# Performance work log

Measured on AMD Instinct MI355X. Metric: run time of the kernel, lower is better.

Reference implementation:

```python
import jax, jax.numpy as jnp
import numpy as np

B, S, E, F, R, T = 2, 2048, 768, 3072, 4, 128
H = 12  # num_heads
HD = E // H
HID = 128  # lora_mlp_dim


def _lin(key, out_f, in_f):
    bound = 1.0 / np.sqrt(in_f)
    return jax.random.uniform(key, (out_f, in_f), jnp.float32, -bound, bound)


def _bias(key, out_f, in_f):
    bound = 1.0 / np.sqrt(in_f)
    return jax.random.uniform(key, (out_f,), jnp.float32, -bound, bound)


def setup_inputs() -> dict:
    key = jax.random.key(0)
    ks = jax.random.split(key, 20)
    return {
        "src": jax.random.normal(ks[0], (B, S, E), jnp.float32),
        "task_embedding": jax.random.normal(ks[1], (B, S, T), jnp.float32),
        "norm1_w": jnp.ones((E,), jnp.float32),
        "norm2_w": jnp.ones((E,), jnp.float32),
        "in_proj_w": _lin(ks[2], 3 * E, E),      # MHA qkv, bias=False
        "out_proj_w": _lin(ks[3], E, E),          # MHA out, bias=False
        "ffn1_w": _lin(ks[4], F, E), "ffn1_b": _bias(ks[5], F, E),
        "ffn2_w": _lin(ks[6], E, F), "ffn2_b": _bias(ks[7], E, F),
        "hA_w1": _lin(ks[8], HID, T), "hA_b1": _bias(ks[9], HID, T),
        "hA_w2": _lin(ks[10], F * R, HID), "hA_b2": _bias(ks[11], F * R, HID),
        "hB_w1": _lin(ks[12], HID, T), "hB_b1": _bias(ks[13], HID, T),
        "hB_w2": _lin(ks[14], R * E, HID), "hB_b2": _bias(ks[15], R * E, HID),
    }


def _rmsnorm(x, w):
    eps = jnp.finfo(x.dtype).eps
    return x * jax.lax.rsqrt(jnp.mean(x * x, axis=-1, keepdims=True) + eps) * w


def reference(src, task_embedding, norm1_w, norm2_w, in_proj_w, out_proj_w,
              ffn1_w, ffn1_b, ffn2_w, ffn2_b,
              hA_w1, hA_b1, hA_w2, hA_b2, hB_w1, hB_b1, hB_w2, hB_b2):
    # --- self-attention block (pre-RMSNorm) ---
    x = _rmsnorm(src, norm1_w)
    qkv = jnp.einsum('bse,fe->bsf', x, in_proj_w)  # [B,S,3E]
    q, k, v = jnp.split(qkv, 3, axis=-1)
    q = q.reshape(B, S, H, HD).transpose(0, 2, 1, 3)
    k = k.reshape(B, S, H, HD).transpose(0, 2, 1, 3)
    v = v.reshape(B, S, H, HD).transpose(0, 2, 1, 3)
    scores = jnp.einsum('bhqd,bhkd->bhqk', q, k) / jnp.sqrt(jnp.float32(HD))
    attn = jax.nn.softmax(scores, axis=-1)
    ctx = jnp.einsum('bhqk,bhkd->bhqd', attn, v)
    ctx = ctx.transpose(0, 2, 1, 3).reshape(B, S, E)
    attn_out = jnp.einsum('bse,fe->bsf', ctx, out_proj_w)
    src = src + attn_out

    # --- FFN block with per-token hypernetwork LoRA on linear1 ---
    x = _rmsnorm(src, norm2_w)
    # hypernetwork: MLP(task) -> per-token A [F,R], B [R,E]
    hA = jax.nn.relu(jnp.einsum('bst,ht->bsh', task_embedding, hA_w1) + hA_b1)
    A_params = (jnp.einsum('bsh,fh->bsf', hA, hA_w2) + hA_b2).reshape(B, S, F, R)
    hB = jax.nn.relu(jnp.einsum('bst,ht->bsh', task_embedding, hB_w1) + hB_b1)
    B_params = (jnp.einsum('bsh,fh->bsf', hB, hB_w2) + hB_b2).reshape(B, S, R, E)

    base = jnp.einsum('bse,fe->bsf', x, ffn1_w) + ffn1_b  # [B,S,F]
    inter = jnp.einsum('bse,bsre->bsr', x, B_params)       # [B,S,R]
    adapt = jnp.einsum('bsr,bsfr->bsf', inter, A_params)   # [B,S,F]
    h = jax.nn.relu(base + adapt)
    out2 = jnp.einsum('bsf,ef->bse', h, ffn2_w) + ffn2_b
    return src + out2
```

## Files before the change

### kernel.cpp

```cpp
#include <hip/hip_runtime.h>
#include <math.h>

#define NB 2
#define NS 2048
#define NE 768
#define NF 3072
#define NHEAD 12
#define NTOK 4096
#define LDW 1344

typedef __bf16 bf16;
typedef __bf16 bf16x4 __attribute__((ext_vector_type(4)));
typedef __bf16 bf16x8 __attribute__((ext_vector_type(8)));
typedef float  f32x4  __attribute__((ext_vector_type(4)));

__device__ __forceinline__ f32x4 mfma_bf16(bf16x8 a, bf16x8 b, f32x4 c) {
  return __builtin_amdgcn_mfma_f32_16x16x32_bf16(a, b, c, 0, 0, 0);
}

__device__ __forceinline__ float fast_exp2(float x) {
#if __has_builtin(__builtin_amdgcn_exp2f)
  return __builtin_amdgcn_exp2f(x);
#else
  return exp2f(x);
#endif
}

__device__ __forceinline__ void glds16(const void* g, void* l) {
  __builtin_amdgcn_global_load_lds((const __attribute__((address_space(1))) void*)g,
                                   (__attribute__((address_space(3))) void*)l,
                                   16, 0, 0);
}

__device__ __forceinline__ void swz_xy(int& bx, int& by) {
  int gx = gridDim.x;
  int i = by*gx + bx;
  int xcd = i & 7, s = i >> 3;
  int bands = gridDim.y >> 3;
  by = xcd*bands + s / gx;
  bx = s % gx;
}

__global__ void prep_kernel(const float* __restrict__ in_proj, const float* __restrict__ out_proj,
                            const float* __restrict__ ffn1_w, const float* __restrict__ ffn1_b,
                            const float* __restrict__ ffn2_w,
                            const float* __restrict__ hA_w1, const float* __restrict__ hA_b1,
                            const float* __restrict__ hA_w2, const float* __restrict__ hA_b2,
                            const float* __restrict__ hB_w1, const float* __restrict__ hB_b1,
                            const float* __restrict__ hB_w2,
                            const float* __restrict__ task,
                            bf16* __restrict__ Wqkv, bf16* __restrict__ Wo, bf16* __restrict__ W2,
                            bf16* __restrict__ W1ab, float* __restrict__ b1ab,
                            bf16* __restrict__ WBp, bf16* __restrict__ Wc,
                            bf16* __restrict__ task_bf)
{
  __shared__ float tb[64*130];
  int stride = gridDim.x * blockDim.x;
  int t0 = blockIdx.x * blockDim.x + threadIdx.x;
  const float QS = 0.125f * 1.44269504088896f;
  for (int i = t0; i < (2304*768)/4; i += stride) {
    float4 v = ((const float4*)in_proj)[i];
    float sc = (i < (768*768)/4) ? QS : 1.0f;
    *(bf16x4*)(Wqkv + i*4) = (bf16x4){(bf16)(v.x*sc), (bf16)(v.y*sc), (bf16)(v.z*sc), (bf16)(v.w*sc)};
  }
  for (int i = t0; i < (768*768)/4; i += stride) {
    float4 v = ((const float4*)out_proj)[i];
    *(bf16x4*)(Wo + i*4) = (bf16x4){(bf16)v.x, (bf16)v.y, (bf16)v.z, (bf16)v.w};
  }
  for (int i = t0; i < (768*3072)/4; i += stride) {
    float4 v = ((const float4*)ffn2_w)[i];
    *(bf16x4*)(W2 + i*4) = (bf16x4){(bf16)v.x, (bf16)v.y, (bf16)v.z, (bf16)v.w};
  }
  for (int i = t0; i < (NTOK*128)/4; i += stride) {
    float4 v = ((const float4*)task)[i];
    *(bf16x4*)(task_bf + i*4) = (bf16x4){(bf16)v.x, (bf16)v.y, (bf16)v.z, (bf16)v.w};
  }
  for (int i = t0; i < 256*128;  i += stride)
    W1ab[i] = (bf16)(i < 128*128 ? hA_w1[i] : hB_w1[i - 128*128]);
  for (int i = t0; i < 256; i += stride) b1ab[i] = (i < 128) ? hA_b1[i] : hB_b1[i-128];

  for (int j0 = blockIdx.x*64; j0 < 3072; j0 += gridDim.x*64) {
    __syncthreads();
    for (int i = threadIdx.x; i < 64*128; i += 256) {
      int jr = i >> 7, hh = i & 127;
      tb[jr*130 + hh] = hB_w2[(long)(j0 + jr)*128 + hh];
    }
    __syncthreads();
    int r = j0 / 768, e0 = j0 % 768;
    for (int i = threadIdx.x; i < 128*64; i += 256) {
      int hh = i >> 6, jr = i & 63;
      WBp[(long)(r*128 + hh)*768 + e0 + jr] = (bf16)tb[jr*130 + hh];
    }
  }

  for (int f = blockIdx.x; f < 3072; f += gridDim.x) {
    const float* hrow = hA_w2 + (long)f*512;
    bf16* wrow = Wc + (long)f*LDW;
    for (int c = threadIdx.x; c < 768; c += 256) wrow[c] = (bf16)ffn1_w[(long)f*768 + c];
    for (int i = threadIdx.x; i < 512; i += 256) {
      int r = i >> 7, h = i & 127;
      wrow[768 + h*4 + r] = (bf16)hrow[i];
    }
    if (threadIdx.x < 4)        wrow[1280 + threadIdx.x] = (bf16)hA_b2[f*4 + threadIdx.x];
    else if (threadIdx.x == 4)  wrow[1284] = (bf16)ffn1_b[f];
    else if (threadIdx.x < 64)  wrow[1280 + threadIdx.x] = (bf16)0.f;
  }
}

__global__ __launch_bounds__(256) void rmsnorm_k(const float* __restrict__ x,
                                                 const float* __restrict__ w,
                                                 bf16* __restrict__ out, int ld_out)
{
  __shared__ float red[4];
  long t = blockIdx.x;
  const float* xr = x + t*NE;
  float ss = 0.f;
  #pragma unroll
  for (int i = 0; i < 3; i++) { float v = xr[threadIdx.x + i*256]; ss += v*v; }
  #pragma unroll
  for (int d = 1; d < 64; d <<= 1) ss += __shfl_xor(ss, d, 64);
  if ((threadIdx.x & 63) == 0) red[threadIdx.x >> 6] = ss;
  __syncthreads();
  float tot = red[0] + red[1] + red[2] + red[3];
  float scale = rsqrtf(tot * (1.f/768.f) + 1.1920928955078125e-07f);
  #pragma unroll
  for (int i = 0; i < 3; i++) {
    int idx = threadIdx.x + i*256;
    out[t*ld_out + idx] = (bf16)(xr[idx] * scale * w[idx]);
  }
}

template<typename OutT, bool RELU, bool BIAS, bool RES>
__global__ __launch_bounds__(256) void gemm_bt_sw(const bf16* __restrict__ A,
                                                  const bf16* __restrict__ Bm,
                                                  OutT* __restrict__ C,
                                                  const float* __restrict__ bias,
                                                  const float* __restrict__ res,
                                                  int K, int lda, int ldb, int ldc)
{
  __shared__ bf16 As[2][128*32];
  __shared__ bf16 Bs[2][128*32];
  const int tid = threadIdx.x;
  int bx = blockIdx.x, by = blockIdx.y;
  swz_xy(bx, by);
  const int m0 = by * 128;
  const int n0 = bx * 128;
  const int w = tid >> 6, lane = tid & 63;
  const int quad = lane >> 4, l16 = lane & 15;
  const int wy = w >> 1, wx = w & 1;

  f32x4 acc[4][4];
  #pragma unroll
  for (int i = 0; i < 4; i++)
    #pragma unroll
    for (int j = 0; j < 4; j++) acc[i][j] = (f32x4){0.f,0.f,0.f,0.f};

  const int i0 = tid, i1 = tid + 256;
  const int R0 = i0 >> 3, cc0 = (i0 & 7) ^ (R0 & 7), r0 = 2*R0 + (cc0 >> 2), ch0 = (cc0 & 3) * 8;
  const int R1 = i1 >> 3, cc1 = (i1 & 7) ^ (R1 & 7), r1 = 2*R1 + (cc1 >> 2), ch1 = (cc1 & 3) * 8;
  const bf16* pA0 = A  + (long)(m0 + r0)*lda + ch0;
  const bf16* pA1 = A  + (long)(m0 + r1)*lda + ch1;
  const bf16* pB0 = Bm + (long)(n0 + r0)*ldb + ch0;
  const bf16* pB1 = Bm + (long)(n0 + r1)*ldb + ch1;
  auto stage = [&](int buf) {
    glds16(pA0, (void*)(&As[buf][i0*8]));
    glds16(pA1, (void*)(&As[buf][i1*8]));
    glds16(pB0, (void*)(&Bs[buf][i0*8]));
    glds16(pB1, (void*)(&Bs[buf][i1*8]));
    pA0 += 32; pA1 += 32; pB0 += 32; pB1 += 32;
  };

  stage(0);
  __builtin_amdgcn_s_waitcnt(0);
  __syncthreads();

  const int Rh = l16 >> 1;
  const int ppq = ((l16 & 1) << 2) | quad;
  const int jfr = ppq ^ Rh;
  const int nsteps = K >> 5;
  for (int s = 0; s < nsteps; ++s) {
    const int cur = s & 1;
    if (s + 1 < nsteps) stage(cur ^ 1);

    bf16x8 af[4], bfr[4];
    #pragma unroll
    for (int mi = 0; mi < 4; ++mi)
      af[mi] = *(const bf16x8*)(&As[cur][(wy*32 + mi*8 + Rh)*64 + jfr*8]);
    #pragma unroll
    for (int ni = 0; ni < 4; ++ni)
      bfr[ni] = *(const bf16x8*)(&Bs[cur][(wx*32 + ni*8 + Rh)*64 + jfr*8]);
    #pragma unroll
    for (int mi = 0; mi < 4; ++mi)
      #pragma unroll
      for (int ni = 0; ni < 4; ++ni)
        acc[mi][ni] = mfma_bf16(af[mi], bfr[ni], acc[mi][ni]);

    __builtin_amdgcn_s_waitcnt(0);
    __syncthreads();
  }

  #pragma unroll
  for (int mi = 0; mi < 4; ++mi)
    #pragma unroll
    for (int ni = 0; ni < 4; ++ni) {
      int col = n0 + wx*64 + ni*16 + l16;
      #pragma unroll
      for (int r = 0; r < 4; ++r) {
        long row = m0 + wy*64 + mi*16 + quad*4 + r;
        float v = acc[mi][ni][r];
        if (BIAS) v += bias[col];
        if (RES)  v += res[row*ldc + col];
        if (RELU) v = v > 0.f ? v : 0.f;
        C[row*ldc + col] = (OutT)v;
      }
    }
}

template<typename OutT, bool RELU, bool BIAS, bool RES>
__global__ __launch_bounds__(256) void gemm64(const bf16* __restrict__ A,
                                              const bf16* __restrict__ Bm,
                                              OutT* __restrict__ C,
                                              const float* __restrict__ bias,
                                              const float* __restrict__ res,
                                              int K, int lda, int ldb, int ldc)
{
  __shared__ bf16 As[2][64*64];
  __shared__ bf16 Bs[2][64*64];
  const int tid = threadIdx.x;
  int bx = blockIdx.x, by = blockIdx.y;
  swz_xy(bx, by);
  const int m0 = by * 64, n0 = bx * 64;
  const int w = tid >> 6, lane = tid & 63;
  const int quad = lane >> 4, l16 = lane & 15;
  const int wy = w >> 1, wx = w & 1;
  const int sw = l16 & 7;

  f32x4 acc[2][2];
  #pragma unroll
  for (int i = 0; i < 2; i++)
    #pragma unroll
    for (int j = 0; j < 2; j++) acc[i][j] = (f32x4){0.f,0.f,0.f,0.f};

  const int c0 = tid, c1 = tid + 256;
  const int r0 = c0 >> 3, g0 = ((c0 & 7) ^ (r0 & 7)) * 8;
  const int r1 = c1 >> 3, g1 = ((c1 & 7) ^ (r1 & 7)) * 8;
  const bf16* pA0 = A  + (long)(m0 + r0)*lda + g0;
  const bf16* pA1 = A  + (long)(m0 + r1)*lda + g1;
  const bf16* pB0 = Bm + (long)(n0 + r0)*ldb + g0;
  const bf16* pB1 = Bm + (long)(n0 + r1)*ldb + g1;
  auto stage = [&](int buf) {
    glds16(pA0, (void*)(&As[buf][c0*8]));
    glds16(pA1, (void*)(&As[buf][c1*8]));
    glds16(pB0, (void*)(&Bs[buf][c0*8]));
    glds16(pB1, (void*)(&Bs[buf][c1*8]));
    pA0 += 64; pA1 += 64; pB0 += 64; pB1 += 64;
  };

  stage(0);
  __builtin_amdgcn_s_waitcnt(0);
  __syncthreads();

  const int nsteps = K >> 6;
  for (int s = 0; s < nsteps; ++s) {
    const int cur = s & 1;
    if (s + 1 < nsteps) stage(cur ^ 1);

    bf16x8 af[2][2], bfr[2][2];
    #pragma unroll
    for (int mi = 0; mi < 2; ++mi)
      #pragma unroll
      for (int kb = 0; kb < 2; ++kb)
        af[mi][kb] = *(const bf16x8*)(&As[cur][(wy*32 + mi*16 + l16)*64 + (((kb*4 + quad) ^ sw))*8]);
    #pragma unroll
    for (int ni = 0; ni < 2; ++ni)
      #pragma unroll
      for (int kb = 0; kb < 2; ++kb)
        bfr[ni][kb] = *(const bf16x8*)(&Bs[cur][(wx*32 + ni*16 + l16)*64 + (((kb*4 + quad) ^ sw))*8]);
    #pragma unroll
    for (int kb = 0; kb < 2; ++kb)
      #pragma unroll
      for (int mi = 0; mi < 2; ++mi)
        #pragma unroll
        for (int ni = 0; ni < 2; ++ni)
          acc[mi][ni] = mfma_bf16(af[mi][kb], bfr[ni][kb], acc[mi][ni]);

    __builtin_amdgcn_s_waitcnt(0);
    __syncthreads();
  }

  #pragma unroll
  for (int mi = 0; mi < 2; ++mi)
    #pragma unroll
    for (int ni = 0; ni < 2; ++ni) {
      int col = n0 + wx*32 + ni*16 + l16;
      #pragma unroll
      for (int r = 0; r < 4; ++r) {
        long row = m0 + wy*32 + mi*16 + quad*4 + r;
        float v = acc[mi][ni][r];
        if (BIAS) v += bias[col];
        if (RES)  v += res[row*ldc + col];
        if (RELU) v = v > 0.f ? v : 0.f;
        C[row*ldc + col] = (OutT)v;
      }
    }
}

__global__ __launch_bounds__(256) void gemm_qkv64(const bf16* __restrict__ A,
                                                  const bf16* __restrict__ Bm,
                                                  bf16* __restrict__ Qkv,
                                                  bf16* __restrict__ Vt)
{
  __shared__ bf16 As[2][64*64];
  __shared__ bf16 Bs[2][64*64];
  const int tid = threadIdx.x;
  int bx = blockIdx.x, by = blockIdx.y;
  swz_xy(bx, by);
  const int m0 = by * 64, n0 = bx * 64;
  const int w = tid >> 6, lane = tid & 63;
  const int quad = lane >> 4, l16 = lane & 15;
  const int wy = w >> 1, wx = w & 1;
  const int sw = l16 & 7;

  f32x4 acc[2][2];
  #pragma unroll
  for (int i = 0; i < 2; i++)
    #pragma unroll
    for (int j = 0; j < 2; j++) acc[i][j] = (f32x4){0.f,0.f,0.f,0.f};

  const int c0 = tid, c1 = tid + 256;
  const int r0 = c0 >> 3, g0 = ((c0 & 7) ^ (r0 & 7)) * 8;
  const int r1 = c1 >> 3, g1 = ((c1 & 7) ^ (r1 & 7)) * 8;
  const bf16* pA0 = A  + (long)(m0 + r0)*768 + g0;
  const bf16* pA1 = A  + (long)(m0 + r1)*768 + g1;
  const bf16* pB0 = Bm + (long)(n0 + r0)*768 + g0;
  const bf16* pB1 = Bm + (long)(n0 + r1)*768 + g1;
  auto stage = [&](int buf) {
    glds16(pA0, (void*)(&As[buf][c0*8]));
    glds16(pA1, (void*)(&As[buf][c1*8]));
    glds16(pB0, (void*)(&Bs[buf][c0*8]));
    glds16(pB1, (void*)(&Bs[buf][c1*8]));
    pA0 += 64; pA1 += 64; pB0 += 64; pB1 += 64;
  };

  stage(0);
  __builtin_amdgcn_s_waitcnt(0);
  __syncthreads();

  for (int s = 0; s < 12; ++s) {
    const int cur = s & 1;
    if (s + 1 < 12) stage(cur ^ 1);

    bf16x8 af[2][2], bfr[2][2];
    #pragma unroll
    for (int mi = 0; mi < 2; ++mi)
      #pragma unroll
      for (int kb = 0; kb < 2; ++kb)
        af[mi][kb] = *(const bf16x8*)(&As[cur][(wy*32 + mi*16 + l16)*64 + (((kb*4 + quad) ^ sw))*8]);
    #pragma unroll
    for (int ni = 0; ni < 2; ++ni)
      #pragma unroll
      for (int kb = 0; kb < 2; ++kb)
        bfr[ni][kb] = *(const bf16x8*)(&Bs[cur][(wx*32 + ni*16 + l16)*64 + (((kb*4 + quad) ^ sw))*8]);
    #pragma unroll
    for (int kb = 0; kb < 2; ++kb)
      #pragma unroll
      for (int mi = 0; mi < 2; ++mi)
        #pragma unroll
        for (int ni = 0; ni < 2; ++ni)
          acc[mi][ni] = mfma_bf16(af[mi][kb], bfr[ni][kb], acc[mi][ni]);

    __builtin_amdgcn_s_waitcnt(0);
    __syncthreads();
  }

  const int bb = m0 >> 11;
  #pragma unroll
  for (int mi = 0; mi < 2; ++mi)
    #pragma unroll
    for (int ni = 0; ni < 2; ++ni) {
      int col = n0 + wx*32 + ni*16 + l16;
      #pragma unroll
      for (int r = 0; r < 4; ++r) {
        long row = m0 + wy*32 + mi*16 + quad*4 + r;
        bf16 v = (bf16)acc[mi][ni][r];
        if (col < 1536) {
          Qkv[row*2304 + col] = v;
        } else {
          int vc = col - 1536;
          int hh = vc >> 6, d = vc & 63;
          long srow = row & (NS-1);
          Vt[((long)(bb*NHEAD + hh)*64 + d)*NS + srow] = v;
        }
      }
    }
}

__global__ __launch_bounds__(128) void flash_attn(const bf16* __restrict__ Qkv,
                                                  const bf16* __restrict__ Vt,
                                                  bf16* __restrict__ Ctx)
{
  __shared__ bf16 Ks[2][64*64];
  __shared__ bf16 Vs[2][64*64];

  const int tid = threadIdx.x;
  const int w = tid >> 6, lane = tid & 63;
  const int quad = lane >> 4, l16 = lane & 15;
  const int bh = blockIdx.y;
  const int b = bh / NHEAD, h = bh % NHEAD;
  const int q0 = blockIdx.x * 64;

  bf16x8 qf[2][2];
  #pragma unroll
  for (int mi = 0; mi < 2; ++mi) {
    const long tq = (long)(b*NS + q0 + w*32 + mi*16 + l16);
    qf[mi][0] = *(const bf16x8*)(Qkv + tq*2304 + h*64 + quad*8);
    qf[mi][1] = *(const bf16x8*)(Qkv + tq*2304 + h*64 + 32 + quad*8);
  }

  bf16x8 ones;
  #pragma unroll
  for (int j = 0; j < 8; ++j) ones[j] = (bf16)1.0f;

  f32x4 o[2][4];
  f32x4 o5[2];
  #pragma unroll
  for (int mi = 0; mi < 2; ++mi) {
    o5[mi] = (f32x4){0.f,0.f,0.f,0.f};
    #pragma unroll
    for (int i = 0; i < 4; i++) o[mi][i] = (f32x4){0.f,0.f,0.f,0.f};
  }

  const bf16* kp[4];
  const bf16* vp[4];
  int cc[4];
  #pragma unroll
  for (int i = 0; i < 4; ++i) {
    int c = tid + i*128;
    cc[i] = c;
    int r = c >> 3, g = ((c & 7) ^ (r & 7)) * 8;
    kp[i] = Qkv + (long)(b*NS + r)*2304 + 768 + h*64 + g;
    vp[i] = Vt + ((long)bh*64 + r)*NS + g;
  }
  auto stage = [&](int buf) {
    #pragma unroll
    for (int i = 0; i < 4; ++i) {
      glds16(kp[i], (void*)(&Ks[buf][cc[i]*8]));
      glds16(vp[i], (void*)(&Vs[buf][cc[i]*8]));
      kp[i] += 64*2304; vp[i] += 64;
    }
  };

  auto body = [&](int cur) {
    bf16x8 kfr[4][2];
    #pragma unroll
    for (int nt = 0; nt < 4; ++nt)
      #pragma unroll
      for (int kb = 0; kb < 2; ++kb)
        kfr[nt][kb] = *(const bf16x8*)(&Ks[cur][(nt*16 + l16)*64 + (((kb*4 + quad) ^ (l16 & 7)))*8]);

    bf16x8 pf[2][2];
    #pragma unroll
    for (int mi = 0; mi < 2; ++mi) {
      f32x4 s[4];
      #pragma unroll
      for (int nt = 0; nt < 4; ++nt) {
        s[nt] = (f32x4){0.f,0.f,0.f,0.f};
        #pragma unroll
        for (int kb = 0; kb < 2; ++kb)
          s[nt] = mfma_bf16(kfr[nt][kb], qf[mi][kb], s[nt]);
      }
      #pragma unroll
      for (int nt = 0; nt < 4; ++nt)
        #pragma unroll
        for (int r = 0; r < 4; ++r)
          pf[mi][nt >> 1][(nt & 1)*4 + r] = (bf16)fast_exp2(s[nt][r]);
    }
    #pragma unroll
    for (int ntp = 0; ntp < 2; ++ntp) {
      bf16x8 vf[4];
      #pragma unroll
      for (int dt = 0; dt < 4; ++dt) {
        int row = dt*16 + l16;
        int cA = ntp*4 + (quad >> 1);
        int base = row*64 + (quad & 1)*4;
        bf16x4 va = *(const bf16x4*)(&Vs[cur][base + ((cA       ^ (row & 7)) << 3)]);
        bf16x4 vb = *(const bf16x4*)(&Vs[cur][base + (((cA + 2) ^ (row & 7)) << 3)]);
        vf[dt] = (bf16x8){va[0],va[1],va[2],va[3], vb[0],vb[1],vb[2],vb[3]};
      }
      #pragma unroll
      for (int mi = 0; mi < 2; ++mi) {
        #pragma unroll
        for (int dt = 0; dt < 4; ++dt)
          o[mi][dt] = mfma_bf16(pf[mi][ntp], vf[dt], o[mi][dt]);
        o5[mi] = mfma_bf16(pf[mi][ntp], ones, o5[mi]);
      }
    }
  };

  stage(0);
  __builtin_amdgcn_s_waitcnt(0);
  __syncthreads();

  for (int t = 0; t < NS/64; t += 2) {
    stage(1);
    body(0);
    __builtin_amdgcn_s_waitcnt(0);
    __syncthreads();
    if (t + 2 < NS/64) stage(0);
    body(1);
    __builtin_amdgcn_s_waitcnt(0);
    __syncthreads();
  }

  #pragma unroll
  for (int mi = 0; mi < 2; ++mi)
    #pragma unroll
    for (int r = 0; r < 4; ++r) {
      float inv = 1.f / o5[mi][r];
      long trow = (long)(b*NS + q0 + w*32 + mi*16 + quad*4 + r);
      #pragma unroll
      for (int dt = 0; dt < 4; ++dt)
        Ctx[trow*NE + h*64 + dt*16 + l16] = (bf16)(o[mi][dt][r] * inv);
    }
}

__global__ __launch_bounds__(256) void build_g(const bf16* __restrict__ HAB,
                                               const float* __restrict__ P,
                                               const float* __restrict__ hB_b2,
                                               bf16* __restrict__ Aext)
{
  long t = blockIdx.x*4 + (threadIdx.x >> 6);
  int lane = threadIdx.x & 63;
  const bf16* xr = Aext + t*LDW;
  float acc[4] = {0.f, 0.f, 0.f, 0.f};
  for (int i = lane; i < 768; i += 64) {
    float xv = (float)xr[i];
    #pragma unroll
    for (int r = 0; r < 4; ++r) acc[r] += xv * hB_b2[r*768 + i];
  }
  const bf16* hB = HAB + t*256 + 128;
  const float* Pr = P + t*512;
  #pragma unroll
  for (int k = 0; k < 2; ++k) {
    int h = lane + k*64;
    float hv = (float)hB[h];
    #pragma unroll
    for (int r = 0; r < 4; ++r) acc[r] += hv * Pr[r*128 + h];
  }
  #pragma unroll
  for (int r = 0; r < 4; ++r)
    #pragma unroll
    for (int d = 1; d < 64; d <<= 1) acc[r] += __shfl_xor(acc[r], d, 64);

  bf16* grow = Aext + t*LDW + 768;
  const bf16* hA = HAB + t*256;
  #pragma unroll
  for (int j = 0; j < 8; ++j) {
    int idx = lane*8 + j;
    int h = idx >> 2, r = idx & 3;
    grow[idx] = (bf16)((float)hA[h] * acc[r]);
  }
  if (lane < 4)       Aext[t*LDW + 1280 + lane] = (bf16)acc[lane];
  else if (lane == 4) Aext[t*LDW + 1284] = (bf16)1.0f;
  else                Aext[t*LDW + 1280 + lane] = (bf16)0.f;
}

extern "C" void kernel_launch(void* const* d_in, const int* in_sizes, int n_in,
                              void* d_out, int out_size, void* d_ws, size_t ws_size,
                              hipStream_t stream)
{
  const float* src      = (const float*)d_in[0];
  const float* task     = (const float*)d_in[1];
  const float* norm1_w  = (const float*)d_in[2];
  const float* norm2_w  = (const float*)d_in[3];
  const float* in_proj  = (const float*)d_in[4];
  const float* out_proj = (const float*)d_in[5];
  const float* ffn1_w   = (const float*)d_in[6];
  const float* ffn1_b   = (const float*)d_in[7];
  const float* ffn2_w   = (const float*)d_in[8];
  const float* ffn2_b   = (const float*)d_in[9];
  const float* hA_w1    = (const float*)d_in[10];
  const float* hA_b1    = (const float*)d_in[11];
  const float* hA_w2    = (const float*)d_in[12];
  const float* hA_b2    = (const float*)d_in[13];
  const float* hB_w1    = (const float*)d_in[14];
  const float* hB_b1    = (const float*)d_in[15];
  const float* hB_w2    = (const float*)d_in[16];
  const float* hB_b2    = (const float*)d_in[17];
  float* out = (float*)d_out;

  char* ws = (char*)d_ws;
  size_t off = 0;
  auto alloc = [&](size_t bytes) { size_t o = off; off += (bytes + 255) & ~(size_t)255; return o; };
  bf16*  Wqkv   = (bf16*)(ws + alloc(2304*768*2));
  bf16*  Wo     = (bf16*)(ws + alloc(768*768*2));
  bf16*  W2     = (bf16*)(ws + alloc(768*3072*2));
  bf16*  W1ab   = (bf16*)(ws + alloc(256*128*2));
  float* b1ab   = (float*)(ws + alloc(256*4));
  bf16*  WBp    = (bf16*)(ws + alloc(512*768*2));
  bf16*  Wc     = (bf16*)(ws + alloc((size_t)3072*LDW*2));
  bf16*  taskbf = (bf16*)(ws + alloc((size_t)NTOK*128*2));
  bf16*  XC     = (bf16*)(ws + alloc((size_t)NTOK*768*2));
  char*  QKVH   = ws + alloc(25165824);
  bf16*  Qkv    = (bf16*)QKVH;
  bf16*  Vt     = (bf16*)(QKVH + 18874368);
  bf16*  Hbuf   = (bf16*)QKVH;
  float* Src2   = (float*)(ws + alloc((size_t)NTOK*768*4));
  bf16*  Aext   = (bf16*)(ws + alloc((size_t)NTOK*LDW*2));
  bf16*  HAB    = (bf16*)(ws + alloc((size_t)NTOK*256*2));
  float* P      = (float*)(ws + alloc((size_t)NTOK*512*4));

  prep_kernel<<<dim3(1280), 256, 0, stream>>>(in_proj, out_proj, ffn1_w, ffn1_b, ffn2_w,
      hA_w1, hA_b1, hA_w2, hA_b2, hB_w1, hB_b1, hB_w2, task,
      Wqkv, Wo, W2, W1ab, b1ab, WBp, Wc, taskbf);
  rmsnorm_k<<<dim3(NTOK), 256, 0, stream>>>(src, norm1_w, XC, 768);
  gemm_qkv64<<<dim3(36,64), 256, 0, stream>>>(XC, Wqkv, Qkv, Vt);
  flash_attn<<<dim3(32,24), 128, 0, stream>>>(Qkv, Vt, XC);
  gemm64<float,false,false,true><<<dim3(12,64), 256, 0, stream>>>(XC, Wo, Src2, nullptr, src, 768, 768, 768, 768);
  rmsnorm_k<<<dim3(NTOK), 256, 0, stream>>>(Src2, norm2_w, Aext, LDW);
  gemm64<bf16,true,true,false><<<dim3(4,64), 256, 0, stream>>>(taskbf, W1ab, HAB, b1ab, nullptr, 128, 128, 128, 256);
  gemm64<float,false,false,false><<<dim3(8,64), 256, 0, stream>>>(Aext, WBp, P, nullptr, nullptr, 768, LDW, 768, 512);
  build_g<<<dim3(NTOK/4), 256, 0, stream>>>(HAB, P, hB_b2, Aext);
  gemm_bt_sw<bf16,true,false,false><<<dim3(24,32), 256, 0, stream>>>(Aext, Wc, Hbuf, nullptr, nullptr, 1312, LDW, LDW, 3072);
  gemm64<float,false,true,true><<<dim3(12,64), 256, 0, stream>>>(Hbuf, W2, out, ffn2_b, Src2, 3072, 3072, 3072, 768);
}
```

Before: 217.9 us.

## Split flash attention KV range across two warp pairs and read V from global

The attention kernel goes from 128 to 256 threads. Two warp pairs each handle half of the key sequence for the same 64 queries, and their partial outputs and row sums are merged through shared memory at the end. V fragments are now loaded straight from global memory in registers instead of being staged through LDS, which halves the shared-memory footprint per pair. A block-index swizzle is also added. This raises parallelism per query tile and occupancy, at the cost of an extra reduction step and non-LDS V loads that may stall.

```diff
diff --git a/kernel.cpp b/kernel.cpp
--- a/kernel.cpp
+++ b/kernel.cpp
@@ -395,24 +395,26 @@
     }
 }
 
-__global__ __launch_bounds__(128) void flash_attn(const bf16* __restrict__ Qkv,
-                                                  const bf16* __restrict__ Vt,
-                                                  bf16* __restrict__ Ctx)
-{
-  __shared__ bf16 Ks[2][64*64];
-  __shared__ bf16 Vs[2][64*64];
+__global__ __launch_bounds__(256, 3) void flash_attn(const bf16* __restrict__ Qkv,
+                                                     const bf16* __restrict__ Vt,
+                                                     bf16* __restrict__ Ctx)
+{
+  __shared__ bf16 Ks[2][2][64*64];
 
   const int tid = threadIdx.x;
   const int w = tid >> 6, lane = tid & 63;
   const int quad = lane >> 4, l16 = lane & 15;
-  const int bh = blockIdx.y;
+  const int pair = w >> 1, qw = w & 1;
+  int bx = blockIdx.x, by = blockIdx.y;
+  swz_xy(bx, by);
+  const int bh = by;
   const int b = bh / NHEAD, h = bh % NHEAD;
-  const int q0 = blockIdx.x * 64;
+  const int q0 = bx * 64;
 
   bf16x8 qf[2][2];
   #pragma unroll
   for (int mi = 0; mi < 2; ++mi) {
-    const long tq = (long)(b*NS + q0 + w*32 + mi*16 + l16);
+    const long tq = (long)(b*NS + q0 + qw*32 + mi*16 + l16);
     qf[mi][0] = *(const bf16x8*)(Qkv + tq*2304 + h*64 + quad*8);
     qf[mi][1] = *(const bf16x8*)(Qkv + tq*2304 + h*64 + 32 + quad*8);
   }
@@ -430,33 +432,38 @@
     for (int i = 0; i < 4; i++) o[mi][i] = (f32x4){0.f,0.f,0.f,0.f};
   }
 
+  const int ptid = tid & 127;
   const bf16* kp[4];
-  const bf16* vp[4];
   int cc[4];
   #pragma unroll
   for (int i = 0; i < 4; ++i) {
-    int c = tid + i*128;
+    int c = ptid + i*128;
     cc[i] = c;
     int r = c >> 3, g = ((c & 7) ^ (r & 7)) * 8;
-    kp[i] = Qkv + (long)(b*NS + r)*2304 + 768 + h*64 + g;
-    vp[i] = Vt + ((long)bh*64 + r)*NS + g;
+    kp[i] = Qkv + (long)(b*NS + pair*1024 + r)*2304 + 768 + h*64 + g;
   }
   auto stage = [&](int buf) {
     #pragma unroll
     for (int i = 0; i < 4; ++i) {
-      glds16(kp[i], (void*)(&Ks[buf][cc[i]*8]));
-      glds16(vp[i], (void*)(&Vs[buf][cc[i]*8]));
-      kp[i] += 64*2304; vp[i] += 64;
+      glds16(kp[i], (void*)(&Ks[pair][buf][cc[i]*8]));
+      kp[i] += (long)64*2304;
     }
   };
 
+  const bf16* vB = Vt + ((long)bh*64 + l16)*NS + pair*1024 + quad*8;
+
   auto body = [&](int cur) {
+    bf16x8 vf0[4];
+    #pragma unroll
+    for (int dt = 0; dt < 4; ++dt)
+      vf0[dt] = *(const bf16x8*)(vB + (long)dt*16*NS);
+
     bf16x8 kfr[4][2];
     #pragma unroll
     for (int nt = 0; nt < 4; ++nt)
       #pragma unroll
       for (int kb = 0; kb < 2; ++kb)
-        kfr[nt][kb] = *(const bf16x8*)(&Ks[cur][(nt*16 + l16)*64 + (((kb*4 + quad) ^ (l16 & 7)))*8]);
+        kfr[nt][kb] = *(const bf16x8*)(&Ks[pair][cur][(nt*16 + l16)*64 + (((kb*4 + quad) ^ (l16 & 7)))*8]);
 
     bf16x8 pf[2][2];
     #pragma unroll
@@ -475,25 +482,26 @@
         for (int r = 0; r < 4; ++r)
           pf[mi][nt >> 1][(nt & 1)*4 + r] = (bf16)fast_exp2(s[nt][r]);
     }
-    #pragma unroll
-    for (int ntp = 0; ntp < 2; ++ntp) {
-      bf16x8 vf[4];
-      #pragma unroll
-      for (int dt = 0; dt < 4; ++dt) {
-        int row = dt*16 + l16;
-        int cA = ntp*4 + (quad >> 1);
-        int base = row*64 + (quad & 1)*4;
-        bf16x4 va = *(const bf16x4*)(&Vs[cur][base + ((cA       ^ (row & 7)) << 3)]);
-        bf16x4 vb = *(const bf16x4*)(&Vs[cur][base + (((cA + 2) ^ (row & 7)) << 3)]);
-        vf[dt] = (bf16x8){va[0],va[1],va[2],va[3], vb[0],vb[1],vb[2],vb[3]};
-      }
-      #pragma unroll
-      for (int mi = 0; mi < 2; ++mi) {
-        #pragma unroll
-        for (int dt = 0; dt < 4; ++dt)
-          o[mi][dt] = mfma_bf16(pf[mi][ntp], vf[dt], o[mi][dt]);
-        o5[mi] = mfma_bf16(pf[mi][ntp], ones, o5[mi]);
-      }
+
+    bf16x8 vf1[4];
+    #pragma unroll
+    for (int dt = 0; dt < 4; ++dt)
+      vf1[dt] = *(const bf16x8*)(vB + (long)dt*16*NS + 32);
+    vB += 64;
+
+    #pragma unroll
+    for (int mi = 0; mi < 2; ++mi) {
+      #pragma unroll
+      for (int dt = 0; dt < 4; ++dt)
+        o[mi][dt] = mfma_bf16(pf[mi][0], vf0[dt], o[mi][dt]);
+      o5[mi] = mfma_bf16(pf[mi][0], ones, o5[mi]);
+    }
+    #pragma unroll
+    for (int mi = 0; mi < 2; ++mi) {
+      #pragma unroll
+      for (int dt = 0; dt < 4; ++dt)
+        o[mi][dt] = mfma_bf16(pf[mi][1], vf1[dt], o[mi][dt]);
+      o5[mi] = mfma_bf16(pf[mi][1], ones, o5[mi]);
     }
   };
 
@@ -501,27 +509,47 @@
   __builtin_amdgcn_s_waitcnt(0);
   __syncthreads();
 
-  for (int t = 0; t < NS/64; t += 2) {
+  for (int t = 0; t < 16; t += 2) {
     stage(1);
     body(0);
     __builtin_amdgcn_s_waitcnt(0);
     __syncthreads();
-    if (t + 2 < NS/64) stage(0);
+    if (t + 2 < 16) stage(0);
     body(1);
     __builtin_amdgcn_s_waitcnt(0);
     __syncthreads();
   }
 
-  #pragma unroll
-  for (int mi = 0; mi < 2; ++mi)
-    #pragma unroll
-    for (int r = 0; r < 4; ++r) {
-      float inv = 1.f / o5[mi][r];
-      long trow = (long)(b*NS + q0 + w*32 + mi*16 + quad*4 + r);
-      #pragma unroll
-      for (int dt = 0; dt < 4; ++dt)
-        Ctx[trow*NE + h*64 + dt*16 + l16] = (bf16)(o[mi][dt][r] * inv);
-    }
+  float* Of = (float*)&Ks[0][0][0];
+  float* Lf = Of + 64*68;
+  const int rbase = qw*32;
+  if (pair == 1) {
+    #pragma unroll
+    for (int mi = 0; mi < 2; ++mi)
+      #pragma unroll
+      for (int r = 0; r < 4; ++r) {
+        int row = rbase + mi*16 + quad*4 + r;
+        if (l16 == 0) Lf[row] = o5[mi][r];
+        #pragma unroll
+        for (int dt = 0; dt < 4; ++dt)
+          Of[row*68 + dt*16 + l16] = o[mi][dt][r];
+      }
+  }
+  __syncthreads();
+  if (pair == 0) {
+    #pragma unroll
+    for (int mi = 0; mi < 2; ++mi)
+      #pragma unroll
+      for (int r = 0; r < 4; ++r) {
+        int row = rbase + mi*16 + quad*4 + r;
+        float inv = 1.f / (o5[mi][r] + Lf[row]);
+        long trow = (long)(b*NS + q0 + row);
+        #pragma unroll
+        for (int dt = 0; dt < 4; ++dt)
+          Ctx[trow*NE + h*64 + dt*16 + l16] =
+            (bf16)((o[mi][dt][r] + Of[row*68 + dt*16 + l16]) * inv);
+      }
+  }
 }
 
 __global__ __launch_bounds__(256) void build_g(const bf16* __restrict__ HAB,
@@ -615,7 +643,7 @@
       Wqkv, Wo, W2, W1ab, b1ab, WBp, Wc, taskbf);
   rmsnorm_k<<<dim3(NTOK), 256, 0, stream>>>(src, norm1_w, XC, 768);
   gemm_qkv64<<<dim3(36,64), 256, 0, stream>>>(XC, Wqkv, Qkv, Vt);
-  flash_attn<<<dim3(32,24), 128, 0, stream>>>(Qkv, Vt, XC);
+  flash_attn<<<dim3(32,24), 256, 0, stream>>>(Qkv, Vt, XC);
   gemm64<float,false,false,true><<<dim3(12,64), 256, 0, stream>>>(XC, Wo, Src2, nullptr, src, 768, 768, 768, 768);
   rmsnorm_k<<<dim3(NTOK), 256, 0, stream>>>(Src2, norm2_w, Aext, LDW);
   gemm64<bf16,true,true,false><<<dim3(4,64), 256, 0, stream>>>(taskbf, W1ab, HAB, b1ab, nullptr, 128, 128, 128, 256);
```

Result: slower. 231.1 us (+6.1%).
